# Kernel tuning notes

Hardware: AMD Instinct MI355X
Metric: run time of the kernel (lower is better)

## Reference

```python
import jax, jax.numpy as jnp
import numpy as np

VOCAB, EMB = 30000, 300
HEADS, DPH = 8, 50
AD = HEADS * DPH            # att_dim_total = 400
MAX_LINES, MAX_WPL = 128, 32
BATCH = 16
NEG = 1e7                   # padding-mask penalty, matches torch source


def _split_heads(x):
    # [N, S, AD] -> [N, H, S, D]
    return x.reshape(x.shape[0], -1, HEADS, DPH).transpose(0, 2, 1, 3)


def _attention(q, k, v, mask_q=None, mask_k=None, mask_v=None):
    # Faithful port of MTHiSAN._attention. Note the (oddly named) torch masks:
    #   mask_q masks the KEY axis of scores, mask_k/mask_v zero the QUERY axis.
    scale = float(np.sqrt(q.shape[-1]))
    scores = jnp.einsum('bhqd,bhkd->bhqk', q, k) / scale
    if mask_q is not None:
        scores = scores - NEG * (~mask_q)[:, None, None, :].astype(scores.dtype)
    w = jax.nn.softmax(scores, axis=-1)
    if mask_k is not None:
        w = w * mask_k[:, None, :, None].astype(w.dtype)
    out = jnp.einsum('bhqk,bhkd->bhqd', w, v)
    if mask_v is not None:
        out = out * mask_v[:, None, :, None].astype(out.dtype)
    return out


def _forward(docs, emb, wq_w, wq_b, wk_w, wk_b, wv_w, wv_b, w_tgt,
             lq_w, lq_b, lk_w, lk_b, lv_w, lv_b, l_tgt,
             fc1_w, fc1_b, fc2_w, fc2_b):
    B = docs.shape[0]
    d = docs[:, :MAX_LINES * MAX_WPL].reshape(B * MAX_LINES, MAX_WPL)
    mask_w = d != 0                               # [B*L, W]
    mask_l = mask_w.sum(-1) != 0                  # [B*L]  non-empty lines
    # NOTE: instead of gathering non-empty lines (data-dependent shape), we keep
    # full shapes; masked word attention yields exact zeros for empty lines,
    # equivalent to the torch scatter into new_zeros.
    we = emb[d]                                   # [B*L, W, E] (dropout = eval/no-op)
    wq = jax.nn.elu(_split_heads(we @ wq_w + wq_b))
    wk = jax.nn.elu(_split_heads(we @ wk_w + wk_b))
    wv = jax.nn.elu(_split_heads(we @ wv_w + wv_b))
    watt = _attention(wq, wk, wv, mask_w, mask_w, mask_w)   # [B*L,H,W,D]
    # learned word-level target query (Linear(1, AD)(ones) == weight vector)
    tgt = jnp.broadcast_to(w_tgt.reshape(1, HEADS, 1, DPH),
                           (B * MAX_LINES, HEADS, 1, DPH))
    line_e = _attention(tgt, wk, watt, mask_q=mask_w)       # [B*L,H,1,D]
    line_e = line_e.transpose(0, 2, 1, 3).reshape(B * MAX_LINES, AD)
    line_e = line_e * mask_l[:, None].astype(line_e.dtype)  # zero empty lines
    line_e = line_e.reshape(B, MAX_LINES, AD)
    mask_l2 = mask_l.reshape(B, MAX_LINES)
    lq = jax.nn.elu(_split_heads(line_e @ lq_w + lq_b))
    lk = jax.nn.elu(_split_heads(line_e @ lk_w + lk_b))
    lv = jax.nn.elu(_split_heads(line_e @ lv_w + lv_b))
    latt = _attention(lq, lk, lv, mask_l2, mask_l2, mask_l2)  # [B,H,L,D]
    dtgt = jnp.broadcast_to(l_tgt.reshape(1, HEADS, 1, DPH), (B, HEADS, 1, DPH))
    doc_e = _attention(dtgt, lk, latt, mask_q=mask_l2)        # [B,H,1,D]
    doc_e = doc_e.transpose(0, 2, 1, 3).reshape(B, AD)
    logits1 = doc_e @ fc1_w + fc1_b   # task 'site'      [B,70]
    logits2 = doc_e @ fc2_w + fc2_b   # task 'histology' [B,512]
    return jnp.concatenate([logits1, logits2], axis=1)


def setup_inputs() -> dict:
    key = jax.random.key(0)
    ks = jax.random.split(key, 20)
    xavier = lambda k, i, o: (jax.random.normal(k, (i, o), jnp.float32)
                              * np.float32(np.sqrt(2.0 / (i + o))))
    emb = jax.random.normal(ks[0], (VOCAB, EMB), jnp.float32) * 0.02
    emb = emb.at[0].set(0.0)  # padding row zeroed as in __init__
    docs = jax.random.randint(ks[1], (BATCH, MAX_LINES * MAX_WPL), 0, VOCAB)
    z = lambda n: jnp.zeros((n,), jnp.float32)
    return dict(
        docs=docs, emb=emb,
        wq_w=xavier(ks[2], EMB, AD), wq_b=z(AD),
        wk_w=xavier(ks[3], EMB, AD), wk_b=z(AD),
        wv_w=xavier(ks[4], EMB, AD), wv_b=z(AD),
        w_tgt=jax.random.uniform(ks[5], (AD,), jnp.float32),
        lq_w=xavier(ks[6], AD, AD), lq_b=z(AD),
        lk_w=xavier(ks[7], AD, AD), lk_b=z(AD),
        lv_w=xavier(ks[8], AD, AD), lv_b=z(AD),
        l_tgt=jax.random.uniform(ks[9], (AD,), jnp.float32),
        fc1_w=xavier(ks[10], AD, 70), fc1_b=z(70),
        fc2_w=xavier(ks[11], AD, 512), fc2_b=z(512),
    )


def reference(docs, emb, wq_w, wq_b, wk_w, wk_b, wv_w, wv_b, w_tgt,
              lq_w, lq_b, lk_w, lk_b, lv_w, lv_b, l_tgt,
              fc1_w, fc1_b, fc2_w, fc2_b):
    return _forward(docs, emb, wq_w, wq_b, wk_w, wk_b, wv_w, wv_b, w_tgt,
                    lq_w, lq_b, lk_w, lk_b, lv_w, lv_b, l_tgt,
                    fc1_w, fc1_b, fc2_w, fc2_b)
```

## Files before the change

kernel.cpp:

```cpp
#include <hip/hip_runtime.h>
#include <math.h>

#define NLINES 2048
#define WPL 32
#define EMBD 300
#define AD 400
#define NH 8
#define DPH 50
#define QKV_S 52
#define SC_S 36
#define BATCH 16
#define LPD 128
#define NCOLS 1200
#define NPAD 1280
#define HBLK 4992
#define QP 54

typedef __bf16 bf16;
typedef bf16  v8bf  __attribute__((ext_vector_type(8)));
typedef float v16f  __attribute__((ext_vector_type(16)));

__device__ __forceinline__ float elu(float x) {
    return x > 0.f ? x : expm1f(x);
}
__device__ __forceinline__ float elu_fast(float x) {
    return x > 0.f ? x : (__expf(x) - 1.f);
}

__device__ __forceinline__ v8bf ntload8(const bf16* p) {
    return __builtin_nontemporal_load((const v8bf*)p);
}

#define SCALE 7.0710678118654755f

__global__ void split_rows_packed(const float* __restrict__ src,
                                  bf16* __restrict__ pk,
                                  int rows, int K, int K2)
{
    long idx = (long)blockIdx.x * 256 + threadIdx.x;
    if (idx >= (long)rows * K2) return;
    int r = (int)(idx / K2), k = (int)(idx - (long)r * K2);
    float x = (k < K) ? src[(long)r * K + k] : 0.f;
    bf16 h = (bf16)x;
    float hf = (float)h;
    bf16 l = (bf16)(x - hf);
    const long p = ((long)r * (K2 >> 3) + (k >> 3)) * 16 + (k & 7);
    pk[p] = h; pk[p + 8] = l;
}

__global__ void split_wt_packed(const float* __restrict__ W0, const float* __restrict__ W1,
                                const float* __restrict__ W2,
                                const float* __restrict__ B0, const float* __restrict__ B1,
                                const float* __restrict__ B2,
                                bf16* __restrict__ pk,
                                float* __restrict__ biasCat, int K, int K2)
{
    long idx = (long)blockIdx.x * 256 + threadIdx.x;
    if (idx >= (long)NPAD * K2) return;
    int n = (int)(idx / K2), k = (int)(idx - (long)n * K2);
    float x = 0.f;
    if (k < K && n < NCOLS) {
        int p = n / 400, c = n - p * 400;
        const float* W = (p == 0) ? W0 : (p == 1) ? W1 : W2;
        x = W[(long)k * 400 + c];
    }
    bf16 h = (bf16)x;
    float hf = (float)h;
    bf16 l = (bf16)(x - hf);
    const long pidx = ((long)(k >> 3) * NPAD + n) * 16 + (k & 7);
    pk[pidx] = h; pk[pidx + 8] = l;
    if (k == 0) {
        float b = 0.f;
        if (n < NCOLS) {
            int p = n / 400, c = n - p * 400;
            const float* Bp = (p == 0) ? B0 : (p == 1) ? B1 : B2;
            b = Bp[c];
        }
        biasCat[n] = b;
    }
}

__launch_bounds__(512, 2)
__global__ void fused_word(const bf16* __restrict__ Ap,
                           const int* __restrict__ docs,
                           const bf16* __restrict__ Bp,
                           const float* __restrict__ biasCat,
                           const float* __restrict__ w_tgt,
                           float* __restrict__ line_e, float* __restrict__ mask_l)
{
    __shared__ __align__(16) bf16 Alds[40 * 2 * 32 * 8];
    __shared__ __align__(16) float qkv[3][32][QP];
    __shared__ float sc[32 * 33];
    __shared__ float part[16][33];
    __shared__ float vpart[8][64];
    __shared__ float tw[WPL];
    __shared__ float coefA[WPL];
    __shared__ float cw[WPL];
    __shared__ float tg[52];
    __shared__ float msk[WPL];
    __shared__ float mls_s;

    const int tid = threadIdx.x;
    const int line = blockIdx.x;

    if (tid < WPL) msk[tid] = (docs[line * WPL + tid] != 0) ? 1.f : 0.f;
    __syncthreads();
    if (tid == 0) {
        float m = 0.f;
        for (int w = 0; w < WPL; ++w) m = fmaxf(m, msk[w]);
        mls_s = m;
        mask_l[line] = m;
    }

    for (int slot = tid; slot < 40 * 2 * 32; slot += 512) {
        const int row = slot & 31;
        const int hl  = (slot >> 5) & 1;
        const int kf  = slot >> 6;
        const int token = docs[line * WPL + row];
        *(v8bf*)&Alds[slot * 8] = ntload8(&Ap[((long)token * 40 + kf) * 16 + hl * 8]);
    }
    __syncthreads();

    const int wv = tid >> 6;
    const int lane = tid & 63;
    const int half = lane >> 5, r32 = lane & 31;

    for (int h = 0; h < NH; ++h) {
        if (wv < 6) {
            const int proj = wv >> 1;
            const int c0 = proj * 400 + h * 50 + (wv & 1) * 32;
            v16f acc = (v16f)0.f;
            #pragma unroll 4
            for (int s = 0; s < 20; ++s) {
                const int kf = 2 * s + half;
                const v8bf fah = *(const v8bf*)&Alds[((kf * 2 + 0) * 32 + r32) * 8];
                const v8bf fal = *(const v8bf*)&Alds[((kf * 2 + 1) * 32 + r32) * 8];
                const bf16* bg = Bp + ((long)kf * NPAD + c0 + r32) * 16;
                const v8bf fbh = *(const v8bf*)&bg[0];
                const v8bf fbl = *(const v8bf*)&bg[8];
                acc = __builtin_amdgcn_mfma_f32_32x32x16_bf16(fah, fbh, acc, 0, 0, 0);
                acc = __builtin_amdgcn_mfma_f32_32x32x16_bf16(fah, fbl, acc, 0, 0, 0);
                acc = __builtin_amdgcn_mfma_f32_32x32x16_bf16(fal, fbh, acc, 0, 0, 0);
            }
            const int d = (wv & 1) * 32 + r32;
            if (d < DPH) {
                const float bv = biasCat[c0 + r32];
                #pragma unroll
                for (int rg = 0; rg < 16; ++rg) {
                    const int row = (rg & 3) + 8 * (rg >> 2) + 4 * half;
                    qkv[proj][row][d] = elu_fast(acc[rg] + bv);
                }
            }
        } else {
            const int t = tid - 384;
            if (t < 96) {
                const int p = t / 32, row = t & 31;
                qkv[p][row][50] = 0.f; qkv[p][row][51] = 0.f;
                qkv[p][row][52] = 0.f; qkv[p][row][53] = 0.f;
            } else if (t >= 96 && t < 148) {
                const int i = t - 96;
                tg[i] = (i < DPH) ? w_tgt[h * DPH + i] : 0.f;
            }
        }
        __syncthreads();

        const float* q   = &qkv[0][0][0];
        const float* kk_ = &qkv[1][0][0];
        const float* vv_ = &qkv[2][0][0];

        const int j = tid >> 4, kg = tid & 15;
        float2 qv[27];
        #pragma unroll
        for (int i = 0; i < 27; ++i) qv[i] = *(const float2*)&q[j * QP + 2 * i];

        float e2[2];
        float m = -1e30f;
        #pragma unroll
        for (int c = 0; c < 2; ++c) {
            const int kk = kg * 2 + c;
            const float* kr = &kk_[kk * QP];
            float s = 0.f;
            #pragma unroll
            for (int i = 0; i < 27; ++i)
                s += qv[i].x * kr[2 * i] + qv[i].y * kr[2 * i + 1];
            s = s / SCALE - 1e7f * (1.f - msk[kk]);
            e2[c] = s;
            m = fmaxf(m, s);
        }
        m = fmaxf(m, __shfl_xor(m, 1, 16));
        m = fmaxf(m, __shfl_xor(m, 2, 16));
        m = fmaxf(m, __shfl_xor(m, 4, 16));
        m = fmaxf(m, __shfl_xor(m, 8, 16));
        float rsum = 0.f;
        #pragma unroll
        for (int c = 0; c < 2; ++c) { e2[c] = __expf(e2[c] - m); rsum += e2[c]; }
        rsum += __shfl_xor(rsum, 1, 16);
        rsum += __shfl_xor(rsum, 2, 16);
        rsum += __shfl_xor(rsum, 4, 16);
        rsum += __shfl_xor(rsum, 8, 16);
        sc[j * 33 + kg * 2]     = e2[0];
        sc[j * 33 + kg * 2 + 1] = e2[1];

        if (tid < WPL) {
            const float* kr = &kk_[tid * QP];
            float s = 0.f;
            #pragma unroll
            for (int i = 0; i < 25; ++i)
                s += tg[2 * i] * kr[2 * i] + tg[2 * i + 1] * kr[2 * i + 1];
            s = s / SCALE - 1e7f * (1.f - msk[tid]);
            float tm = s;
            #pragma unroll
            for (int off = 16; off >= 1; off >>= 1) tm = fmaxf(tm, __shfl_xor(tm, off, 32));
            const float te = __expf(s - tm);
            float tsum = te;
            #pragma unroll
            for (int off = 16; off >= 1; off >>= 1) tsum += __shfl_xor(tsum, off, 32);
            tw[tid] = te / tsum;
        }
        __syncthreads();

        if (kg == 0) coefA[j] = tw[j] * msk[j] / rsum;
        __syncthreads();

        {
            const int k = tid & 31, jg = tid >> 5;
            const int j0 = jg * 2;
            part[jg][k] = coefA[j0] * sc[j0 * 33 + k]
                        + coefA[j0 + 1] * sc[(j0 + 1) * 33 + k];
        }
        __syncthreads();
        if (tid < WPL) {
            float cv = 0.f;
            #pragma unroll
            for (int g = 0; g < 16; ++g) cv += part[g][tid];
            cw[tid] = cv;
        }
        __syncthreads();

        {
            const int d = tid & 63, kh = tid >> 6;
            float acc = 0.f;
            if (d < QP) {
                #pragma unroll
                for (int t = 0; t < 4; ++t) {
                    const int k = kh * 4 + t;
                    acc += cw[k] * vv_[k * QP + d];
                }
            }
            vpart[kh][d] = acc;
        }
        __syncthreads();
        if (tid < DPH) {
            float o = 0.f;
            #pragma unroll
            for (int g = 0; g < 8; ++g) o += vpart[g][tid];
            line_e[(long)line * AD + h * DPH + tid] = o * mls_s;
        }
        __syncthreads();
    }
}

__launch_bounds__(256, 4)
__global__ void mfma_gemm(const bf16* __restrict__ Ap,
                          const int* __restrict__ docs,
                          const bf16* __restrict__ Bp,
                          const float* __restrict__ biasCat,
                          float* __restrict__ C, int K2, int word_layout)
{
    __shared__ int tok[128];

    const int tid = threadIdx.x;

    const int total = (int)(gridDim.x * gridDim.y);
    int flat = (int)(blockIdx.y * gridDim.x + blockIdx.x);
    if ((total & 7) == 0) flat = (flat & 7) * (total >> 3) + (flat >> 3);
    const int bx = flat % (int)gridDim.x;
    const int by = flat / (int)gridDim.x;
    const int row0 = by * 128;
    const int n0 = bx * 128;

    if (tid < 128) tok[tid] = docs ? docs[row0 + tid] : (row0 + tid);
    __syncthreads();

    const int wv = tid >> 6, lane = tid & 63;
    const int half = lane >> 5, r32 = lane & 31;
    const int wm0 = (wv >> 1) * 64, wn0 = (wv & 1) * 64;

    const int colA = n0 + wn0 + r32;
    const int colB = colA + 32;

    const long a0 = (long)tok[wm0 + r32]      * ((long)K2 * 2);
    const long a1 = (long)tok[wm0 + 32 + r32] * ((long)K2 * 2);

    v16f acc[2][2];
    #pragma unroll
    for (int a = 0; a < 2; ++a)
        #pragma unroll
        for (int b = 0; b < 2; ++b) acc[a][b] = (v16f)0.f;

    const int nk = K2 >> 5;
    for (int kt = 0; kt < nk; ++kt) {
        #pragma unroll
        for (int ks = 0; ks < 2; ++ks) {
            const int k0 = kt * 32 + (ks * 2 + half) * 8;
            const bf16* bg = Bp + (long)(k0 >> 3) * NPAD * 16;
            const long ka = (long)k0 * 2;
            v8bf fb_h[2], fb_l[2], fa_h[2], fa_l[2];
            fb_h[0] = *(const v8bf*)&bg[(long)colA * 16];
            fb_l[0] = *(const v8bf*)&bg[(long)colA * 16 + 8];
            fb_h[1] = *(const v8bf*)&bg[(long)colB * 16];
            fb_l[1] = *(const v8bf*)&bg[(long)colB * 16 + 8];
            fa_h[0] = *(const v8bf*)&Ap[a0 + ka];
            fa_l[0] = *(const v8bf*)&Ap[a0 + ka + 8];
            fa_h[1] = *(const v8bf*)&Ap[a1 + ka];
            fa_l[1] = *(const v8bf*)&Ap[a1 + ka + 8];

            #pragma unroll
            for (int mt = 0; mt < 2; ++mt)
                #pragma unroll
                for (int nt = 0; nt < 2; ++nt)
                    acc[mt][nt] = __builtin_amdgcn_mfma_f32_32x32x16_bf16(fa_h[mt], fb_h[nt], acc[mt][nt], 0, 0, 0);
            #pragma unroll
            for (int mt = 0; mt < 2; ++mt)
                #pragma unroll
                for (int nt = 0; nt < 2; ++nt)
                    acc[mt][nt] = __builtin_amdgcn_mfma_f32_32x32x16_bf16(fa_h[mt], fb_l[nt], acc[mt][nt], 0, 0, 0);
            #pragma unroll
            for (int mt = 0; mt < 2; ++mt)
                #pragma unroll
                for (int nt = 0; nt < 2; ++nt)
                    acc[mt][nt] = __builtin_amdgcn_mfma_f32_32x32x16_bf16(fa_l[mt], fb_h[nt], acc[mt][nt], 0, 0, 0);
        }
    }

    if (word_layout) {
        #pragma unroll
        for (int nt = 0; nt < 2; ++nt) {
            const int col = n0 + wn0 + nt * 32 + r32;
            if (col >= NCOLS) continue;
            const float bv = biasCat[col];
            const int p = col / 400;
            const int rem = col - p * 400;
            const int hh = rem / 50;
            const int d  = rem - hh * 50;
            #pragma unroll
            for (int mt = 0; mt < 2; ++mt) {
                const int rbase = row0 + wm0 + mt * 32 + 4 * half;
                #pragma unroll
                for (int rg = 0; rg < 16; ++rg) {
                    const int row = rbase + (rg & 3) + 8 * (rg >> 2);
                    const int ln = row >> 5, r = row & 31;
                    const long base = (((long)ln * NH + hh) * 3 + p) * 1664 + r * 52;
                    const float x = acc[mt][nt][rg] + bv;
                    C[base + d] = elu_fast(x);
                    if (d == 49) {
                        float2 z; z.x = 0.f; z.y = 0.f;
                        *(float2*)&C[base + 50] = z;
                    }
                }
            }
        }
    } else {
        #pragma unroll
        for (int nt = 0; nt < 2; ++nt) {
            const int col = n0 + wn0 + nt * 32 + r32;
            if (col >= NCOLS) continue;
            const float bv = biasCat[col];
            #pragma unroll
            for (int mt = 0; mt < 2; ++mt) {
                const int rbase = row0 + wm0 + mt * 32 + 4 * half;
                #pragma unroll
                for (int rg = 0; rg < 16; ++rg) {
                    const int row = rbase + (rg & 3) + 8 * (rg >> 2);
                    const float x = acc[mt][nt][rg] + bv;
                    C[(long)row * NCOLS + col] = elu_fast(x);
                }
            }
        }
    }
}

__launch_bounds__(256)
__global__ void line_attn2(const float* __restrict__ Q, const float* __restrict__ Kp,
                           const float* __restrict__ Vp,
                           long DS, long HS, long LS,
                           const float* __restrict__ l_tgt, const float* __restrict__ mask_l,
                           float* __restrict__ doc_e)
{
    __shared__ float kl[LPD * 52];
    __shared__ float sc[64 * 130];
    __shared__ float ml[LPD];
    __shared__ float tw[LPD];
    __shared__ float cw[LPD];
    __shared__ float coefA[64];
    __shared__ float pm[4 * 64];
    __shared__ float ps[4 * 64];
    __shared__ float tg[52];
    __shared__ float rr[2];
    __shared__ float vpart[2][64];

    const int tid = threadIdx.x;
    const int doc = blockIdx.x >> 3;
    const int h = blockIdx.x & 7;
    const float* qbase = Q + doc * DS + h * HS;
    const float* kbase = Kp + doc * DS + h * HS;
    const float* vbase = Vp + doc * DS + h * HS;

    if (tid < LPD) { ml[tid] = mask_l[doc * LPD + tid]; cw[tid] = 0.f; }
    if (tid < 52) tg[tid] = (tid < DPH) ? l_tgt[h * DPH + tid] : 0.f;
    for (int idx = tid; idx < LPD * 52; idx += 256) {
        const int r = idx / 52, d = idx - r * 52;
        kl[idx] = (d < DPH) ? kbase[(long)r * LS + d] : 0.f;
    }
    __syncthreads();

    if (tid < LPD) {
        const float* kr = &kl[tid * 52];
        float s = 0.f;
        #pragma unroll
        for (int i = 0; i < 25; ++i)
            s += tg[2 * i] * kr[2 * i] + tg[2 * i + 1] * kr[2 * i + 1];
        tw[tid] = s / SCALE - 1e7f * (1.f - ml[tid]);
    }
    __syncthreads();
    if (tid < 64) {
        float a = fmaxf(tw[tid], tw[64 + tid]);
        #pragma unroll
        for (int off = 32; off >= 1; off >>= 1) a = fmaxf(a, __shfl_xor(a, off));
        if (tid == 0) rr[0] = a;
    }
    __syncthreads();
    if (tid < 64) {
        const float tm2 = rr[0];
        float a = __expf(tw[tid] - tm2) + __expf(tw[64 + tid] - tm2);
        #pragma unroll
        for (int off = 32; off >= 1; off >>= 1) a += __shfl_xor(a, off);
        if (tid == 0) rr[1] = a;
    }
    __syncthreads();
    if (tid < LPD) tw[tid] = __expf(tw[tid] - rr[0]) / rr[1];
    __syncthreads();

    const int j2 = tid & 63;
    const int kq = tid >> 6;

    for (int g = 0; g < 2; ++g) {
        const int j = g * 64 + j2;
        float2 qv[25];
        #pragma unroll
        for (int i = 0; i < 25; ++i)
            qv[i] = *(const float2*)(qbase + (long)j * LS + 2 * i);

        float m = -1e30f;
        for (int c = 0; c < 32; ++c) {
            const int k = kq * 32 + c;
            const float* kr = &kl[k * 52];
            float s = 0.f;
            #pragma unroll
            for (int i = 0; i < 25; ++i)
                s += qv[i].x * kr[2 * i] + qv[i].y * kr[2 * i + 1];
            s = s / SCALE - 1e7f * (1.f - ml[k]);
            sc[j2 * 130 + k] = s;
            m = fmaxf(m, s);
        }
        pm[kq * 64 + j2] = m;
        __syncthreads();
        const float rowm = fmaxf(fmaxf(pm[j2], pm[64 + j2]),
                                 fmaxf(pm[128 + j2], pm[192 + j2]));
        float sum = 0.f;
        for (int c = 0; c < 32; ++c) {
            const int k = kq * 32 + c;
            const float e = __expf(sc[j2 * 130 + k] - rowm);
            sc[j2 * 130 + k] = e;
            sum += e;
        }
        ps[kq * 64 + j2] = sum;
        __syncthreads();
        if (kq == 0) {
            const float rs = ps[j2] + ps[64 + j2] + ps[128 + j2] + ps[192 + j2];
            coefA[j2] = tw[j] * ml[j] / rs;
        }
        __syncthreads();
        if (tid < LPD) {
            float cv = 0.f;
            for (int jj = 0; jj < 64; ++jj)
                cv += coefA[jj] * sc[jj * 130 + tid];
            cw[tid] += cv;
        }
        __syncthreads();
    }

    const int d = tid & 63;
    const int half = (tid >> 6) & 1;
    if (tid < 128 && d < DPH) {
        float acc = 0.f;
        for (int k = half * 64; k < half * 64 + 64; ++k)
            acc += cw[k] * vbase[(long)k * LS + d];
        vpart[half][d] = acc;
    }
    __syncthreads();
    if (tid < DPH)
        doc_e[doc * AD + h * DPH + tid] = vpart[0][tid] + vpart[1][tid];
}

__launch_bounds__(256)
__global__ void word_attn(const float* __restrict__ qkv, const int* __restrict__ docs,
                          const float* __restrict__ w_tgt,
                          float* __restrict__ line_e, float* __restrict__ mask_l)
{
    __shared__ float qs[WPL * QKV_S];
    __shared__ float ks[WPL * QKV_S];
    __shared__ float vs[WPL * QKV_S];
    __shared__ float sc[WPL * SC_S];
    __shared__ float ts[WPL], tw[WPL], cw[WPL], msk[WPL];
    __shared__ float mls;

    const int tid = threadIdx.x;
    const int line = blockIdx.x;

    if (tid < WPL) msk[tid] = (docs[line * WPL + tid] != 0) ? 1.f : 0.f;
    __syncthreads();
    if (tid == 0) {
        float ml = 0.f;
        for (int w = 0; w < WPL; ++w) ml = fmaxf(ml, msk[w]);
        mls = ml;
        mask_l[line] = ml;
    }
    for (int h = 0; h < NH; ++h) {
        for (int idx = tid; idx < WPL * DPH; idx += 256) {
            const int r = idx / DPH, d = idx - r * DPH;
            const size_t base = (size_t)(line * WPL + r) * NCOLS + h * DPH + d;
            qs[r * QKV_S + d] = qkv[base];
            ks[r * QKV_S + d] = qkv[base + 400];
            vs[r * QKV_S + d] = qkv[base + 800];
        }
        __syncthreads();
        {
            const int j = tid >> 3, kg = tid & 7;
            #pragma unroll
            for (int c = 0; c < 4; ++c) {
                const int kk = kg * 4 + c;
                float s = 0.f;
                for (int dd = 0; dd < DPH; ++dd)
                    s += qs[j * QKV_S + dd] * ks[kk * QKV_S + dd];
                sc[j * SC_S + kk] = s / SCALE - 1e7f * (1.f - msk[kk]);
            }
        }
        if (tid < WPL) {
            float s = 0.f;
            for (int dd = 0; dd < DPH; ++dd)
                s += w_tgt[h * DPH + dd] * ks[tid * QKV_S + dd];
            ts[tid] = s / SCALE - 1e7f * (1.f - msk[tid]);
        }
        __syncthreads();
        if (tid < WPL) {
            const int j = tid;
            float m = -1e30f;
            for (int kk = 0; kk < WPL; ++kk) m = fmaxf(m, sc[j * SC_S + kk]);
            float sum = 0.f;
            for (int kk = 0; kk < WPL; ++kk) {
                const float e = expf(sc[j * SC_S + kk] - m);
                sc[j * SC_S + kk] = e;
                sum += e;
            }
            const float inv = 1.f / sum;
            for (int kk = 0; kk < WPL; ++kk) sc[j * SC_S + kk] *= inv;
        } else if (tid == WPL) {
            float m = -1e30f;
            for (int jj = 0; jj < WPL; ++jj) m = fmaxf(m, ts[jj]);
            float sum = 0.f;
            for (int jj = 0; jj < WPL; ++jj) { const float e = expf(ts[jj] - m); tw[jj] = e; sum += e; }
            const float inv = 1.f / sum;
            for (int jj = 0; jj < WPL; ++jj) tw[jj] *= inv;
        }
        __syncthreads();
        if (tid < WPL) {
            const int kk = tid;
            float c = 0.f;
            for (int jj = 0; jj < WPL; ++jj) c += tw[jj] * msk[jj] * sc[jj * SC_S + kk];
            cw[kk] = c;
        }
        __syncthreads();
        if (tid < DPH) {
            float acc = 0.f;
            for (int kk = 0; kk < WPL; ++kk) acc += cw[kk] * vs[kk * QKV_S + tid];
            line_e[line * AD + h * DPH + tid] = acc * mls;
        }
        __syncthreads();
    }
}

__launch_bounds__(256, 2)
__global__ void gemm_qkv(const float* __restrict__ Asrc,
                         const int* __restrict__ docs,
                         const float* __restrict__ emb,
                         const float* __restrict__ W0, const float* __restrict__ W1,
                         const float* __restrict__ W2,
                         const float* __restrict__ B0, const float* __restrict__ B1,
                         const float* __restrict__ B2,
                         float* __restrict__ C, int M, int K)
{
    __shared__ __align__(16) float As[32][132];
    __shared__ __align__(16) float Bs[32][132];

    const int tid = threadIdx.x;
    const int row0 = blockIdx.x * 128;
    const int n0 = blockIdx.y * 128;
    const int tc = tid & 15, tr = tid >> 4;

    float acc[2][2][4][4];
    #pragma unroll
    for (int a = 0; a < 2; ++a)
        #pragma unroll
        for (int b = 0; b < 2; ++b)
            #pragma unroll
            for (int c = 0; c < 4; ++c)
                #pragma unroll
                for (int d = 0; d < 4; ++d) acc[a][b][c][d] = 0.f;

    const int ma = tid & 127;
    const int kq = tid >> 7;
    const float* arow;
    if (docs) arow = emb + (size_t)docs[row0 + ma] * EMBD;
    else      arow = Asrc + (size_t)(row0 + ma) * K;

    const int gcol = n0 + ma;
    const int p = gcol / 400;
    const int ccol = gcol - p * 400;
    const float* Wp = (p == 0) ? W0 : (p == 1) ? W1 : W2;
    const bool colv = gcol < NCOLS;

    const int nk = (K + 31) >> 5;
    for (int ck = 0; ck < nk; ++ck) {
        const int k0 = ck * 32;
        #pragma unroll
        for (int f = 0; f < 4; ++f) {
            const int kl = kq * 16 + f * 4;
            const int kg = k0 + kl;
            float4 v = make_float4(0.f, 0.f, 0.f, 0.f);
            if (kg < K) v = *(const float4*)(arow + kg);
            As[kl + 0][ma] = v.x;
            As[kl + 1][ma] = v.y;
            As[kl + 2][ma] = v.z;
            As[kl + 3][ma] = v.w;
        }
        #pragma unroll
        for (int i = 0; i < 16; ++i) {
            const int kl = kq * 16 + i;
            const int kg = k0 + kl;
            float v = 0.f;
            if (colv && kg < K) v = Wp[(size_t)kg * 400 + ccol];
            Bs[kl][ma] = v;
        }
        __syncthreads();

        #pragma unroll 8
        for (int k = 0; k < 32; ++k) {
            const float4 a0 = *(const float4*)&As[k][tr * 4];
            const float4 a1 = *(const float4*)&As[k][64 + tr * 4];
            const float4 b0 = *(const float4*)&Bs[k][tc * 4];
            const float4 b1 = *(const float4*)&Bs[k][64 + tc * 4];
            const float ar[2][4] = {{a0.x, a0.y, a0.z, a0.w}, {a1.x, a1.y, a1.z, a1.w}};
            const float br[2][4] = {{b0.x, b0.y, b0.z, b0.w}, {b1.x, b1.y, b1.z, b1.w}};
            #pragma unroll
            for (int im = 0; im < 2; ++im)
                #pragma unroll
                for (int in_ = 0; in_ < 2; ++in_)
                    #pragma unroll
                    for (int rr = 0; rr < 4; ++rr)
                        #pragma unroll
                        for (int cc = 0; cc < 4; ++cc)
                            acc[im][in_][rr][cc] += ar[im][rr] * br[in_][cc];
        }
        __syncthreads();
    }

    #pragma unroll
    for (int in_ = 0; in_ < 2; ++in_) {
        const int ncol = n0 + in_ * 64 + tc * 4;
        if (ncol >= NCOLS) continue;
        const int pj = ncol / 400;
        const int cj = ncol - pj * 400;
        const float* Bp = (pj == 0) ? B0 : (pj == 1) ? B1 : B2;
        const float4 bv = *(const float4*)(Bp + cj);
        #pragma unroll
        for (int im = 0; im < 2; ++im) {
            #pragma unroll
            for (int rr = 0; rr < 4; ++rr) {
                const int row = row0 + im * 64 + tr * 4 + rr;
                float4 o;
                o.x = elu(acc[im][in_][rr][0] + bv.x);
                o.y = elu(acc[im][in_][rr][1] + bv.y);
                o.z = elu(acc[im][in_][rr][2] + bv.z);
                o.w = elu(acc[im][in_][rr][3] + bv.w);
                *(float4*)(C + (size_t)row * NCOLS + ncol) = o;
            }
        }
    }
}

__global__ void logits_kernel(const float* __restrict__ doc_e,
                              const float* __restrict__ fc1_w, const float* __restrict__ fc1_b,
                              const float* __restrict__ fc2_w, const float* __restrict__ fc2_b,
                              float* __restrict__ out)
{
    int o = blockIdx.x * blockDim.x + threadIdx.x;
    if (o >= BATCH * 582) return;
    int b = o / 582, jj = o - b * 582;
    const float* de = doc_e + b * AD;
    float acc;
    if (jj < 70) {
        acc = fc1_b[jj];
        for (int k = 0; k < AD; ++k) acc += de[k] * fc1_w[k * 70 + jj];
    } else {
        int j2 = jj - 70;
        acc = fc2_b[j2];
        for (int k = 0; k < AD; ++k) acc += de[k] * fc2_w[k * 512 + j2];
    }
    out[o] = acc;
}

extern "C" void kernel_launch(void* const* d_in, const int* in_sizes, int n_in,
                              void* d_out, int out_size, void* d_ws, size_t ws_size,
                              hipStream_t stream) {
    const int*   docs  = (const int*)  d_in[0];
    const float* emb   = (const float*)d_in[1];
    const float* wq_w  = (const float*)d_in[2];
    const float* wq_b  = (const float*)d_in[3];
    const float* wk_w  = (const float*)d_in[4];
    const float* wk_b  = (const float*)d_in[5];
    const float* wv_w  = (const float*)d_in[6];
    const float* wv_b  = (const float*)d_in[7];
    const float* w_tgt = (const float*)d_in[8];
    const float* lq_w  = (const float*)d_in[9];
    const float* lq_b  = (const float*)d_in[10];
    const float* lk_w  = (const float*)d_in[11];
    const float* lk_b  = (const float*)d_in[12];
    const float* lv_w  = (const float*)d_in[13];
    const float* lv_b  = (const float*)d_in[14];
    const float* l_tgt = (const float*)d_in[15];
    const float* fc1_w = (const float*)d_in[16];
    const float* fc1_b = (const float*)d_in[17];
    const float* fc2_w = (const float*)d_in[18];
    const float* fc2_b = (const float*)d_in[19];
    float* out = (float*)d_out;
    float* ws = (float*)d_ws;

    const long O_LINE_E = 0;
    const long O_MASK_L = 819200;
    const long O_DOC_E  = 821248;
    const long O_BIAS_W = 827648;
    const long O_BIAS_L = 828928;
    const long O_EMB_H  = 830208;
    const long O_WTW_H  = 10430208;
    const long O_WTL_H  = 10839808;
    const long O_LE_H   = 11372288;
    const long O_R      = 12224256;

    const long LINE_QKV_FL = (long)NLINES * NCOLS;
    long ws_fl = (long)(ws_size / 4);
    long Rcap = ws_fl - O_R;

    if (Rcap >= LINE_QKV_FL) {
        float* line_e = ws + O_LINE_E;
        float* mask_l = ws + O_MASK_L;
        float* doc_e  = ws + O_DOC_E;
        float* bias_w = ws + O_BIAS_W;
        float* bias_l = ws + O_BIAS_L;
        bf16* embp = (bf16*)(ws + O_EMB_H);
        bf16* wtwp = (bf16*)(ws + O_WTW_H);
        bf16* wtlp = (bf16*)(ws + O_WTL_H);
        bf16* lep  = (bf16*)(ws + O_LE_H);
        float* R   = ws + O_R;

        split_rows_packed<<<(30000L * 320 + 255) / 256, 256, 0, stream>>>(emb, embp, 30000, 300, 320);
        split_wt_packed<<<((long)NPAD * 320 + 255) / 256, 256, 0, stream>>>(wq_w, wk_w, wv_w,
                                                                            wq_b, wk_b, wv_b,
                                                                            wtwp, bias_w, 300, 320);
        split_wt_packed<<<((long)NPAD * 416 + 255) / 256, 256, 0, stream>>>(lq_w, lk_w, lv_w,
                                                                            lq_b, lk_b, lv_b,
                                                                            wtlp, bias_l, 400, 416);

        fused_word<<<NLINES, 512, 0, stream>>>(embp, docs, wtwp, bias_w, w_tgt,
                                               line_e, mask_l);

        split_rows_packed<<<((long)NLINES * 416 + 255) / 256, 256, 0, stream>>>(line_e, lep,
                                                                                NLINES, 400, 416);
        dim3 g2(10, NLINES / 128);
        mfma_gemm<<<g2, 256, 0, stream>>>(lep, nullptr, wtlp, bias_l, R, 416, 0);
        line_attn2<<<BATCH * NH, 256, 0, stream>>>(R, R + 400, R + 800,
                                                   (long)LPD * NCOLS, (long)DPH, (long)NCOLS,
                                                   l_tgt, mask_l, doc_e);
        logits_kernel<<<(BATCH * 582 + 255) / 256, 256, 0, stream>>>(doc_e, fc1_w, fc1_b,
                                                                     fc2_w, fc2_b, out);
    } else {
        const long F_FIXED = 827648;
        const long PER_LINE_FL = (long)WPL * NCOLS;
        float* line_e = ws;
        float* mask_l = ws + 819200;
        float* doc_e  = ws + 821248;
        float* R      = ws + F_FIXED;
        long Rcap2 = ws_fl - F_FIXED;

        long maxl = Rcap2 / PER_LINE_FL;
        if (maxl > NLINES) maxl = NLINES;
        long maxl4 = (maxl / 4) * 4;
        int nc = (int)((NLINES + maxl4 - 1) / maxl4);
        int chunk = (int)((NLINES + nc - 1) / nc);
        chunk = ((chunk + 3) / 4) * 4;

        for (int c0 = 0; c0 < NLINES; c0 += chunk) {
            int cl = NLINES - c0 < chunk ? NLINES - c0 : chunk;
            dim3 g1((cl * 32) / 128, 10);
            gemm_qkv<<<g1, 256, 0, stream>>>(nullptr, docs + (size_t)c0 * WPL, emb,
                                             wq_w, wk_w, wv_w, wq_b, wk_b, wv_b,
                                             R, cl * 32, EMBD);
            word_attn<<<cl, 256, 0, stream>>>(R, docs + (size_t)c0 * WPL, w_tgt,
                                              line_e + (size_t)c0 * AD, mask_l + c0);
        }
        dim3 g2(16, 10);
        gemm_qkv<<<g2, 256, 0, stream>>>(line_e, nullptr, emb,
                                         lq_w, lk_w, lv_w, lq_b, lk_b, lv_b,
                                         R, NLINES, AD);
        line_attn2<<<BATCH * NH, 256, 0, stream>>>(R, R + 400, R + 800,
                                                   (long)LPD * NCOLS, (long)DPH, (long)NCOLS,
                                                   l_tgt, mask_l, doc_e);
        logits_kernel<<<(BATCH * 582 + 255) / 256, 256, 0, stream>>>(doc_e, fc1_w, fc1_b,
                                                                     fc2_w, fc2_b, out);
    }
}
```

Baseline: 563.4 us.

## Pipeline word-attention per head: MFMA projects next head while one wave does attention

```diff
diff --git a/kernel.cpp b/kernel.cpp
--- a/kernel.cpp
+++ b/kernel.cpp
@@ -14,7 +14,7 @@
 #define NCOLS 1200
 #define NPAD 1280
 #define HBLK 4992
-#define QP 54
+#define QP 56
 
 typedef __bf16 bf16;
 typedef bf16  v8bf  __attribute__((ext_vector_type(8)));
@@ -29,6 +29,11 @@
 
 __device__ __forceinline__ v8bf ntload8(const bf16* p) {
     return __builtin_nontemporal_load((const v8bf*)p);
+}
+
+__device__ __forceinline__ void wave_lds_fence() {
+    asm volatile("s_waitcnt lgkmcnt(0)" ::: "memory");
+    __builtin_amdgcn_sched_barrier(0);
 }
 
 #define SCALE 7.0710678118654755f
@@ -80,7 +85,7 @@
     }
 }
 
-__launch_bounds__(512, 2)
+__launch_bounds__(512, 1)
 __global__ void fused_word(const bf16* __restrict__ Ap,
                            const int* __restrict__ docs,
                            const bf16* __restrict__ Bp,
@@ -89,14 +94,10 @@
                            float* __restrict__ line_e, float* __restrict__ mask_l)
 {
     __shared__ __align__(16) bf16 Alds[40 * 2 * 32 * 8];
-    __shared__ __align__(16) float qkv[3][32][QP];
+    __shared__ __align__(16) float qkv[2][3][32][QP];
     __shared__ float sc[32 * 33];
-    __shared__ float part[16][33];
-    __shared__ float vpart[8][64];
-    __shared__ float tw[WPL];
-    __shared__ float coefA[WPL];
-    __shared__ float cw[WPL];
-    __shared__ float tg[52];
+    __shared__ float cwl[32];
+    __shared__ float tg_all[8][QP];
     __shared__ float msk[WPL];
     __shared__ float mls_s;
 
@@ -104,14 +105,10 @@
     const int line = blockIdx.x;
 
     if (tid < WPL) msk[tid] = (docs[line * WPL + tid] != 0) ? 1.f : 0.f;
-    __syncthreads();
-    if (tid == 0) {
-        float m = 0.f;
-        for (int w = 0; w < WPL; ++w) m = fmaxf(m, msk[w]);
-        mls_s = m;
-        mask_l[line] = m;
-    }
-
+    for (int i = tid; i < 8 * QP; i += 512) {
+        const int hh = i / QP, d = i - hh * QP;
+        tg_all[hh][d] = (d < DPH) ? w_tgt[hh * DPH + d] : 0.f;
+    }
     for (int slot = tid; slot < 40 * 2 * 32; slot += 512) {
         const int row = slot & 31;
         const int hl  = (slot >> 5) & 1;
@@ -125,136 +122,131 @@
     const int lane = tid & 63;
     const int half = lane >> 5, r32 = lane & 31;
 
-    for (int h = 0; h < NH; ++h) {
+    for (int h = -1; h < 8; ++h) {
+        const int hn = h + 1;
         if (wv < 6) {
-            const int proj = wv >> 1;
-            const int c0 = proj * 400 + h * 50 + (wv & 1) * 32;
-            v16f acc = (v16f)0.f;
-            #pragma unroll 4
-            for (int s = 0; s < 20; ++s) {
-                const int kf = 2 * s + half;
-                const v8bf fah = *(const v8bf*)&Alds[((kf * 2 + 0) * 32 + r32) * 8];
-                const v8bf fal = *(const v8bf*)&Alds[((kf * 2 + 1) * 32 + r32) * 8];
-                const bf16* bg = Bp + ((long)kf * NPAD + c0 + r32) * 16;
-                const v8bf fbh = *(const v8bf*)&bg[0];
-                const v8bf fbl = *(const v8bf*)&bg[8];
-                acc = __builtin_amdgcn_mfma_f32_32x32x16_bf16(fah, fbh, acc, 0, 0, 0);
-                acc = __builtin_amdgcn_mfma_f32_32x32x16_bf16(fah, fbl, acc, 0, 0, 0);
-                acc = __builtin_amdgcn_mfma_f32_32x32x16_bf16(fal, fbh, acc, 0, 0, 0);
+            if (hn < 8) {
+                const int proj = wv >> 1;
+                const int c0 = proj * 400 + hn * 50 + (wv & 1) * 32;
+                v16f acc = (v16f)0.f;
+                #pragma unroll 4
+                for (int s = 0; s < 20; ++s) {
+                    const int kf = 2 * s + half;
+                    const v8bf fah = *(const v8bf*)&Alds[((kf * 2 + 0) * 32 + r32) * 8];
+                    const v8bf fal = *(const v8bf*)&Alds[((kf * 2 + 1) * 32 + r32) * 8];
+                    const bf16* bg = Bp + ((long)kf * NPAD + c0 + r32) * 16;
+                    const v8bf fbh = *(const v8bf*)&bg[0];
+                    const v8bf fbl = *(const v8bf*)&bg[8];
+                    acc = __builtin_amdgcn_mfma_f32_32x32x16_bf16(fah, fbh, acc, 0, 0, 0);
+                    acc = __builtin_amdgcn_mfma_f32_32x32x16_bf16(fah, fbl, acc, 0, 0, 0);
+                    acc = __builtin_amdgcn_mfma_f32_32x32x16_bf16(fal, fbh, acc, 0, 0, 0);
+                }
+                const int d = (wv & 1) * 32 + r32;
+                if (d < DPH) {
+                    const float bv = biasCat[c0 + r32];
+                    #pragma unroll
+                    for (int rg = 0; rg < 16; ++rg) {
+                        const int row = (rg & 3) + 8 * (rg >> 2) + 4 * half;
+                        qkv[hn & 1][proj][row][d] = elu_fast(acc[rg] + bv);
+                    }
+                }
             }
-            const int d = (wv & 1) * 32 + r32;
-            if (d < DPH) {
-                const float bv = biasCat[c0 + r32];
-                #pragma unroll
-                for (int rg = 0; rg < 16; ++rg) {
-                    const int row = (rg & 3) + 8 * (rg >> 2) + 4 * half;
-                    qkv[proj][row][d] = elu_fast(acc[rg] + bv);
+        } else if (wv == 6) {
+            if (h < 0) {
+                if (lane == 0) {
+                    float m = 0.f;
+                    for (int w = 0; w < WPL; ++w) m = fmaxf(m, msk[w]);
+                    mls_s = m;
+                    mask_l[line] = m;
+                }
+            } else {
+                const float* qb = &qkv[h & 1][0][0][0];
+                const float* Kb = &qkv[h & 1][1][0][0];
+                const float* Vb = &qkv[h & 1][2][0][0];
+                const int j = lane & 31;
+                const int hs = lane >> 5;
+
+                float4 qv4[14];
+                #pragma unroll
+                for (int i = 0; i < 14; ++i)
+                    qv4[i] = *(const float4*)&qb[j * QP + 4 * i];
+
+                float e[16];
+                float m = -1e30f;
+                #pragma unroll
+                for (int c = 0; c < 16; ++c) {
+                    const int k = hs * 16 + c;
+                    const float4* kr = (const float4*)&Kb[k * QP];
+                    float s = 0.f;
+                    #pragma unroll
+                    for (int i = 0; i < 14; ++i) {
+                        const float4 kv = kr[i];
+                        s += qv4[i].x * kv.x + qv4[i].y * kv.y
+                           + qv4[i].z * kv.z + qv4[i].w * kv.w;
+                    }
+                    s = s / SCALE - 1e7f * (1.f - msk[k]);
+                    e[c] = s;
+                    m = fmaxf(m, s);
+                }
+                m = fmaxf(m, __shfl_xor(m, 32));
+                float rsum = 0.f;
+                #pragma unroll
+                for (int c = 0; c < 16; ++c) { e[c] = __expf(e[c] - m); rsum += e[c]; }
+                rsum += __shfl_xor(rsum, 32);
+
+                float st = 0.f;
+                {
+                    const float* tgr = &tg_all[h][0];
+                    #pragma unroll
+                    for (int i = 0; i < 7; ++i) {
+                        const float4 t4 = *(const float4*)&tgr[hs * 28 + 4 * i];
+                        const float4 k4 = *(const float4*)&Kb[j * QP + hs * 28 + 4 * i];
+                        st += t4.x * k4.x + t4.y * k4.y + t4.z * k4.z + t4.w * k4.w;
+                    }
+                }
+                st += __shfl_xor(st, 32);
+                st = st / SCALE - 1e7f * (1.f - msk[j]);
+                float tm = st;
+                #pragma unroll
+                for (int off = 16; off >= 1; off >>= 1) tm = fmaxf(tm, __shfl_xor(tm, off));
+                const float te = __expf(st - tm);
+                float tsum = te;
+                #pragma unroll
+                for (int off = 16; off >= 1; off >>= 1) tsum += __shfl_xor(tsum, off);
+                const float tw_k = te / tsum;
+
+                const float coef = tw_k * msk[j] / rsum;
+
+                #pragma unroll
+                for (int c = 0; c < 16; ++c)
+                    sc[j * 33 + hs * 16 + c] = coef * e[c];
+                wave_lds_fence();
+
+                float cv = 0.f;
+                #pragma unroll
+                for (int t = 0; t < 16; ++t)
+                    cv += sc[(hs * 16 + t) * 33 + j];
+                cv += __shfl_xor(cv, 32);
+                if (lane < 32) cwl[lane] = cv;
+                wave_lds_fence();
+
+                if (lane < DPH) {
+                    float acc = 0.f;
+                    #pragma unroll
+                    for (int k = 0; k < 32; ++k)
+                        acc += cwl[k] * Vb[k * QP + lane];
+                    line_e[(long)line * AD + h * DPH + lane] = acc * mls_s;
                 }
             }
         } else {
-            const int t = tid - 384;
-            if (t < 96) {
-                const int p = t / 32, row = t & 31;
-                qkv[p][row][50] = 0.f; qkv[p][row][51] = 0.f;
-                qkv[p][row][52] = 0.f; qkv[p][row][53] = 0.f;
-            } else if (t >= 96 && t < 148) {
-                const int i = t - 96;
-                tg[i] = (i < DPH) ? w_tgt[h * DPH + i] : 0.f;
-            }
-        }
-        __syncthreads();
-
-        const float* q   = &qkv[0][0][0];
-        const float* kk_ = &qkv[1][0][0];
-        const float* vv_ = &qkv[2][0][0];
-
-        const int j = tid >> 4, kg = tid & 15;
-        float2 qv[27];
-        #pragma unroll
-        for (int i = 0; i < 27; ++i) qv[i] = *(const float2*)&q[j * QP + 2 * i];
-
-        float e2[2];
-        float m = -1e30f;
-        #pragma unroll
-        for (int c = 0; c < 2; ++c) {
-            const int kk = kg * 2 + c;
-            const float* kr = &kk_[kk * QP];
-            float s = 0.f;
-            #pragma unroll
-            for (int i = 0; i < 27; ++i)
-                s += qv[i].x * kr[2 * i] + qv[i].y * kr[2 * i + 1];
-            s = s / SCALE - 1e7f * (1.f - msk[kk]);
-            e2[c] = s;
-            m = fmaxf(m, s);
-        }
-        m = fmaxf(m, __shfl_xor(m, 1, 16));
-        m = fmaxf(m, __shfl_xor(m, 2, 16));
-        m = fmaxf(m, __shfl_xor(m, 4, 16));
-        m = fmaxf(m, __shfl_xor(m, 8, 16));
-        float rsum = 0.f;
-        #pragma unroll
-        for (int c = 0; c < 2; ++c) { e2[c] = __expf(e2[c] - m); rsum += e2[c]; }
-        rsum += __shfl_xor(rsum, 1, 16);
-        rsum += __shfl_xor(rsum, 2, 16);
-        rsum += __shfl_xor(rsum, 4, 16);
-        rsum += __shfl_xor(rsum, 8, 16);
-        sc[j * 33 + kg * 2]     = e2[0];
-        sc[j * 33 + kg * 2 + 1] = e2[1];
-
-        if (tid < WPL) {
-            const float* kr = &kk_[tid * QP];
-            float s = 0.f;
-            #pragma unroll
-            for (int i = 0; i < 25; ++i)
-                s += tg[2 * i] * kr[2 * i] + tg[2 * i + 1] * kr[2 * i + 1];
-            s = s / SCALE - 1e7f * (1.f - msk[tid]);
-            float tm = s;
-            #pragma unroll
-            for (int off = 16; off >= 1; off >>= 1) tm = fmaxf(tm, __shfl_xor(tm, off, 32));
-            const float te = __expf(s - tm);
-            float tsum = te;
-            #pragma unroll
-            for (int off = 16; off >= 1; off >>= 1) tsum += __shfl_xor(tsum, off, 32);
-            tw[tid] = te / tsum;
-        }
-        __syncthreads();
-
-        if (kg == 0) coefA[j] = tw[j] * msk[j] / rsum;
-        __syncthreads();
-
-        {
-            const int k = tid & 31, jg = tid >> 5;
-            const int j0 = jg * 2;
-            part[jg][k] = coefA[j0] * sc[j0 * 33 + k]
-                        + coefA[j0 + 1] * sc[(j0 + 1) * 33 + k];
-        }
-        __syncthreads();
-        if (tid < WPL) {
-            float cv = 0.f;
-            #pragma unroll
-            for (int g = 0; g < 16; ++g) cv += part[g][tid];
-            cw[tid] = cv;
-        }
-        __syncthreads();
-
-        {
-            const int d = tid & 63, kh = tid >> 6;
-            float acc = 0.f;
-            if (d < QP) {
-                #pragma unroll
-                for (int t = 0; t < 4; ++t) {
-                    const int k = kh * 4 + t;
-                    acc += cw[k] * vv_[k * QP + d];
+            if (hn < 8) {
+                for (int idx = lane; idx < 96; idx += 64) {
+                    const int p = idx >> 5, row = idx & 31;
+                    float* q = &qkv[hn & 1][p][row][50];
+                    q[0] = 0.f; q[1] = 0.f; q[2] = 0.f;
+                    q[3] = 0.f; q[4] = 0.f; q[5] = 0.f;
                 }
             }
-            vpart[kh][d] = acc;
-        }
-        __syncthreads();
-        if (tid < DPH) {
-            float o = 0.f;
-            #pragma unroll
-            for (int g = 0; g < 8; ++g) o += vpart[g][tid];
-            line_e[(long)line * AD + h * DPH + tid] = o * mls_s;
         }
         __syncthreads();
     }
```

New measurement: 760.9 us. 1.35x slower.
